# Kernel optimization log

Hardware: AMD Instinct MI355X
Metric: run time of the kernel (lower is better)

The kernel has to match this reference:

```python
import jax, jax.numpy as jnp
import numpy as np

# Hard-coded 36-node detector graph from the source (1-indexed), 220 directed edges.
E_SRC = [1,2,3,4,5,6,7,8,9,10,11,12,13,14,15,16,17,18,19,20,21,22,23,24,25,26,27,28,29,30,31,32,33,34,35,36,4,3,8,7,19,20,15,16,35,36,31,32,11,12,11,11,11,12,12,12,6,5,25,26,28,25,9,9,9,10,10,10,1,2,3,4,5,6,7,8,9,10,11,12,13,14,15,16,17,18,17,18,19,20,16,15,31,32,36,35,3,4,7,8,6,5,25,28,14,9,12,11,1,4,2,3,4,1,6,7,8,5,10,11,12,9,14,15,16,13,18,19,20,17,22,23,24,21,26,27,28,25,30,31,32,29,34,35,36,33,33,34,1,2,14,13,30,29,23,22,21,24,22,21,36,33,4,31,30,15,27,28,18,17,10,9,14,19,18,5,8,1,19,20,21,22,23,24,25,26,27,28,29,30,31,32,33,34,35,36,25,26,13,14,30,29,24,21,23,22,33,34,1,2,28,27,10,9,12,15,22,21,11,10]
E_DST = [2,3,4,1,6,7,8,5,10,11,12,9,14,15,16,13,18,19,20,17,22,23,24,21,26,27,28,25,30,31,32,29,34,35,36,33,33,34,1,2,14,13,30,29,23,22,21,24,22,21,36,33,4,31,30,15,27,28,18,17,10,9,14,19,18,5,8,1,19,20,21,22,23,24,25,26,27,28,29,30,31,32,33,34,35,36,25,26,13,14,30,29,24,21,23,22,33,34,1,2,28,27,10,9,12,15,22,21,11,10,1,2,3,4,5,6,7,8,9,10,11,12,13,14,15,16,17,18,19,20,21,22,23,24,25,26,27,28,29,30,31,32,33,34,35,36,4,3,8,7,19,20,15,16,35,36,31,32,11,12,11,11,11,12,12,12,6,5,25,26,28,25,9,9,9,10,10,10,1,2,3,4,5,6,7,8,9,10,11,12,13,14,15,16,17,18,17,18,19,20,16,15,31,32,36,35,3,4,7,8,6,5,25,28,14,9,12,11,1,4]

B = 20000   # graphs per batch
P = 36      # nodes per graph
N = B * P


def setup_inputs() -> dict:
    key = jax.random.key(0)
    ks = jax.random.split(key, 12)
    src = np.asarray(E_SRC, np.int32) - 1
    dst = np.asarray(E_DST, np.int32) - 1
    offs = (np.arange(B, dtype=np.int32) * P)[:, None]
    edge_index = jnp.asarray(np.stack([(src[None, :] + offs).reshape(-1),
                                       (dst[None, :] + offs).reshape(-1)]))  # [2, B*220]
    batch_index = jnp.asarray(np.repeat(np.arange(B, dtype=np.int32), P))  # [N]
    x = jax.random.normal(ks[0], (N, 2), jnp.float32)
    pos = jax.random.normal(ks[1], (N, 3), jnp.float32)  # unused by forward (faithful to source)

    def lin_w(k, fi, fo):
        s = 1.0 / np.sqrt(fi)
        return jax.random.uniform(k, (fi, fo), jnp.float32, -s, s)

    def lin_b(k, fo):
        return jax.random.uniform(k, (fo,), jnp.float32, -0.05, 0.05)

    return {
        "x": x, "edge_index": edge_index, "pos": pos, "batch_index": batch_index,
        "W0": lin_w(ks[2], 2, 4),   "b0": lin_b(ks[3], 4),
        "W1": lin_w(ks[4], 4, 12),  "b1": lin_b(ks[5], 12),
        "W2": lin_w(ks[6], 12, 16), "b2": lin_b(ks[7], 16),
        "W3": lin_w(ks[8], 16, 32), "b3": lin_b(ks[9], 32),
        "Wfc": lin_w(ks[10], 64, 7), "bfc": lin_b(ks[11], 7),
    }


def reference(x, edge_index, pos, batch_index, W0, b0, W1, b1, W2, b2, W3, b3, Wfc, bfc):
    del pos  # present in the torch signature but unused
    src, dst = edge_index[0], edge_index[1]
    n = x.shape[0]
    # GCN symmetric normalization with self-loops: deg = 1 + in-degree
    deg = jax.ops.segment_sum(jnp.ones(src.shape, x.dtype), dst, num_segments=n) + 1.0
    inv = deg ** -0.5
    enorm = inv[src] * inv[dst]   # edge norm
    snorm = inv * inv             # self-loop norm (deg^-1)

    def gcn_conv(h, W, b):
        h = h @ W  # [n, fo]
        agg = jax.ops.segment_sum(h[src] * enorm[:, None], dst, num_segments=n)
        return agg + h * snorm[:, None] + b

    h = jax.nn.relu(gcn_conv(x, W0, b0))
    h = jax.nn.relu(gcn_conv(h, W1, b1))
    # dropout(0.2) is identity in eval mode
    h = jax.nn.relu(gcn_conv(h, W2, b2))
    h = jax.nn.relu(gcn_conv(h, W3, b3))

    gmp = jax.ops.segment_max(h, batch_index, num_segments=B)
    counts = jax.ops.segment_sum(jnp.ones((n,), h.dtype), batch_index, num_segments=B)
    gap = jax.ops.segment_sum(h, batch_index, num_segments=B) / counts[:, None]
    hidden = jnp.concatenate([gmp, gap], axis=1)  # [B, 64]
    out = jax.nn.relu(hidden @ Wfc + bfc)         # [B, 7]
    return (out, hidden)
```

## Files before the change

### kernel.cpp

```cpp
#include <hip/hip_runtime.h>

typedef __attribute__((ext_vector_type(2))) float f32x2;
typedef __attribute__((ext_vector_type(4))) float f32x4;

#define NGRAPH 20000
#define GPT 7
#define STRIDE 36
#define SB (STRIDE * 4)
#define BSTREAM (GPT * 36 * STRIDE)
#define BSTREAMB (BSTREAM * 4)

static __constant__ int c_indeg[36] = {
    7,5,5,7,6,5,5,6,9,9,9,9,5,7,7,5,5,6,6,5,7,7,5,5,7,5,5,7,5,6,6,5,6,5,5,6
};
static __constant__ signed char c_adj[36][9] = {
    {3,7,9,6,1,18,10,0,0},      {0,6,7,2,19,0,0,0,0},
    {1,3,33,32,20,0,0,0,0},     {2,10,0,32,21,33,9,0,0},
    {7,9,5,27,22,26,0,0,0},     {4,6,26,23,27,0,0,0,0},
    {5,7,1,24,0,0,0,0,0},       {6,9,4,0,25,1,0,0,0},
    {11,24,27,9,13,18,17,26,14},{8,27,24,3,10,4,7,0,27},
    {9,0,11,21,35,32,3,28,20},  {10,13,8,20,30,29,14,29,21},
    {15,19,18,13,30,0,0,0,0},   {12,18,8,19,14,31,11,0,0},
    {13,11,8,15,29,32,28,0,0},  {14,12,28,33,29,0,0,0,0},
    {19,25,17,34,24,0,0,0,0},   {16,24,8,18,35,25,0,0,0},
    {17,8,0,19,13,12,0,0,0},    {18,1,16,12,13,0,0,0,0},
    {23,30,11,2,31,10,21,0,0},  {20,35,10,3,34,11,22,0,0},
    {21,34,4,35,23,0,0,0,0},    {22,31,5,30,20,0,0,0,0},
    {27,6,16,25,17,8,9,0,0},    {24,7,17,26,16,0,0,0,0},
    {25,5,8,27,4,0,0,0,0},      {26,4,9,5,24,9,8,0,0},
    {31,15,10,14,29,0,0,0,0},   {28,14,11,11,15,30,0,0,0},
    {29,11,12,31,20,23,0,0,0},  {30,13,28,23,20,0,0,0,0},
    {35,3,10,14,2,33,0,0,0},    {32,2,15,3,34,0,0,0,0},
    {33,16,35,22,21,0,0,0,0},   {34,10,17,32,21,22,0,0,0},
};
static __constant__ float c_inv[36] = {
    0.35355339f,0.40824829f,0.40824829f,0.35355339f,0.37796447f,0.40824829f,
    0.40824829f,0.37796447f,0.31622777f,0.31622777f,0.31622777f,0.31622777f,
    0.40824829f,0.35355339f,0.35355339f,0.40824829f,0.40824829f,0.37796447f,
    0.37796447f,0.40824829f,0.35355339f,0.35355339f,0.40824829f,0.40824829f,
    0.35355339f,0.40824829f,0.40824829f,0.35355339f,0.40824829f,0.37796447f,
    0.37796447f,0.40824829f,0.37796447f,0.40824829f,0.40824829f,0.37796447f,
};

static __device__ __forceinline__ f32x2 relu2(f32x2 v) {
    return __builtin_elementwise_max(v, (f32x2){0.f, 0.f});
}

static __device__ __forceinline__ void xf1(const float* a, const float* W1,
                                           const float* b1, f32x2* h) {
    f32x2 z[6];
    const f32x2* bv = (const f32x2*)b1;
#pragma unroll
    for (int j = 0; j < 6; ++j) z[j] = bv[j];
    const f32x2* Wv = (const f32x2*)W1;
#pragma unroll
    for (int i = 0; i < 4; ++i) {
        const f32x2 av = {a[i], a[i]};
#pragma unroll
        for (int j = 0; j < 6; ++j)
            z[j] = __builtin_elementwise_fma(av, Wv[i * 6 + j], z[j]);
    }
#pragma unroll
    for (int j = 0; j < 6; ++j) h[j] = relu2(z[j]);
}
static __device__ __forceinline__ void xf2(const float* a, const float* W2,
                                           const float* b2, f32x2* h) {
    f32x2 z[8];
    const f32x2* bv = (const f32x2*)b2;
#pragma unroll
    for (int j = 0; j < 8; ++j) z[j] = bv[j];
    const f32x2* Wv = (const f32x2*)W2;
#pragma unroll
    for (int i = 0; i < 12; ++i) {
        const f32x2 av = {a[i], a[i]};
#pragma unroll
        for (int j = 0; j < 8; ++j)
            z[j] = __builtin_elementwise_fma(av, Wv[i * 8 + j], z[j]);
    }
#pragma unroll
    for (int j = 0; j < 8; ++j) h[j] = relu2(z[j]);
}
static __device__ __forceinline__ void xf3(const float* a, const float* W3,
                                           const float* b3, f32x2* h) {
    f32x2 z[16];
    const f32x2* bv = (const f32x2*)b3;
#pragma unroll
    for (int j = 0; j < 16; ++j) z[j] = bv[j];
    const f32x2* Wv = (const f32x2*)W3;
#pragma unroll
    for (int i = 0; i < 16; ++i) {
        const f32x2 av = {a[i], a[i]};
#pragma unroll
        for (int j = 0; j < 16; ++j)
            z[j] = __builtin_elementwise_fma(av, Wv[i * 16 + j], z[j]);
    }
#pragma unroll
    for (int j = 0; j < 16; ++j) h[j] = relu2(z[j]);
}

extern "C" __global__ __launch_bounds__(256, 2)
void gcn_fused(const float* __restrict__ x,
               const float* __restrict__ W0, const float* __restrict__ b0,
               const float* __restrict__ W1, const float* __restrict__ b1,
               const float* __restrict__ W2, const float* __restrict__ b2,
               const float* __restrict__ W3, const float* __restrict__ b3,
               const float* __restrict__ Wfc, const float* __restrict__ bfc,
               float* __restrict__ out)
{
    __shared__ float L[2 * BSTREAM];

    const int t = threadIdx.x;
    const int g = t / 36;
    const int v = t - g * 36;
    const bool act = (g < GPT);
    const int gq = act ? g : GPT - 1;
    const int vc = act ? v : 0;
    const int GA = blockIdx.x * (2 * GPT) + g;
    const int GB = GA + GPT;
    const int GcA = (act && GA < NGRAPH) ? GA : 0;
    const int GcB = (act && GB < NGRAPH) ? GB : 0;
    const bool okB = (GB < NGRAPH);

    const int nd = c_indeg[vc];
    const float inv_v = c_inv[vc];
    int aoff[9], boff[9];
#pragma unroll
    for (int k = 0; k < 9; ++k) {
        aoff[k] = (gq * 36 + (int)c_adj[vc][k]) * SB;
        boff[k] = aoff[k] + BSTREAMB;
    }
    float* srowA = &L[(gq * 36 + vc) * STRIDE];
    float* srowB = srowA + BSTREAM;
    const char* Lb = (const char*)L;

    f32x2 h0A[2], h0B[2];
    {
        const float2* x2 = (const float2*)x;
        const float2 xA = x2[(size_t)GcA * 36 + vc];
        const float2 xB = x2[(size_t)GcB * 36 + vc];
        const f32x2 sA = {xA.x * inv_v, xA.y * inv_v};
        const f32x2 sB = {xB.x * inv_v, xB.y * inv_v};
        if (act) { *(f32x2*)&srowA[32] = sA; *(f32x2*)&srowB[32] = sB; }
        __syncthreads();
        f32x2 cA = sA, cB = sB;
#pragma unroll
        for (int k = 0; k < 5; ++k) {
            cA += *(const f32x2*)(Lb + aoff[k] + 128);
            cB += *(const f32x2*)(Lb + boff[k] + 128);
        }
        if (nd > 5) { cA += *(const f32x2*)(Lb + aoff[5] + 128);
                      cB += *(const f32x2*)(Lb + boff[5] + 128); }
        if (nd > 6) { cA += *(const f32x2*)(Lb + aoff[6] + 128);
                      cB += *(const f32x2*)(Lb + boff[6] + 128); }
        if (nd > 7) { cA += *(const f32x2*)(Lb + aoff[7] + 128);
                      cB += *(const f32x2*)(Lb + boff[7] + 128);
                      cA += *(const f32x2*)(Lb + aoff[8] + 128);
                      cB += *(const f32x2*)(Lb + boff[8] + 128); }
        const f32x2* W0v = (const f32x2*)W0;
        const f32x2* b0v = (const f32x2*)b0;
        {
            const float a0 = cA.x * inv_v, a1 = cA.y * inv_v;
            const f32x2 a0v = {a0, a0}, a1v = {a1, a1};
            h0A[0] = relu2(__builtin_elementwise_fma(a0v, W0v[0],
                     __builtin_elementwise_fma(a1v, W0v[2], b0v[0])));
            h0A[1] = relu2(__builtin_elementwise_fma(a0v, W0v[1],
                     __builtin_elementwise_fma(a1v, W0v[3], b0v[1])));
        }
        {
            const float a0 = cB.x * inv_v, a1 = cB.y * inv_v;
            const f32x2 a0v = {a0, a0}, a1v = {a1, a1};
            h0B[0] = relu2(__builtin_elementwise_fma(a0v, W0v[0],
                     __builtin_elementwise_fma(a1v, W0v[2], b0v[0])));
            h0B[1] = relu2(__builtin_elementwise_fma(a0v, W0v[1],
                     __builtin_elementwise_fma(a1v, W0v[3], b0v[1])));
        }
    }

    f32x2 h1A[6], h1B[6];
    {
        const f32x2 iv = {inv_v, inv_v};
        const f32x2 sA0 = h0A[0] * iv, sA1 = h0A[1] * iv;
        const f32x2 sB0 = h0B[0] * iv, sB1 = h0B[1] * iv;
        if (act) {
            *(f32x4*)&srowA[0] = (f32x4){sA0.x, sA0.y, sA1.x, sA1.y};
            *(f32x4*)&srowB[0] = (f32x4){sB0.x, sB0.y, sB1.x, sB1.y};
        }
        __syncthreads();
        f32x4 cA = {sA0.x, sA0.y, sA1.x, sA1.y};
        f32x4 cB = {sB0.x, sB0.y, sB1.x, sB1.y};
#pragma unroll
        for (int k = 0; k < 5; ++k) {
            cA += *(const f32x4*)(Lb + aoff[k]);
            cB += *(const f32x4*)(Lb + boff[k]);
        }
        if (nd > 5) { cA += *(const f32x4*)(Lb + aoff[5]);
                      cB += *(const f32x4*)(Lb + boff[5]); }
        if (nd > 6) { cA += *(const f32x4*)(Lb + aoff[6]);
                      cB += *(const f32x4*)(Lb + boff[6]); }
        if (nd > 7) { cA += *(const f32x4*)(Lb + aoff[7]);
                      cB += *(const f32x4*)(Lb + boff[7]);
                      cA += *(const f32x4*)(Lb + aoff[8]);
                      cB += *(const f32x4*)(Lb + boff[8]); }
        float aA[4], aB[4];
#pragma unroll
        for (int i = 0; i < 4; ++i) { aA[i] = cA[i] * inv_v; aB[i] = cB[i] * inv_v; }
        xf1(aA, W1, b1, h1A);
        xf1(aB, W1, b1, h1B);
    }

    f32x2 h2A[8], h2B[8];
    {
        const f32x2 iv = {inv_v, inv_v};
        f32x2 sA[6], sB[6];
#pragma unroll
        for (int j = 0; j < 6; ++j) { sA[j] = h1A[j] * iv; sB[j] = h1B[j] * iv; }
        if (act) {
            *(f32x4*)&srowA[4]  = (f32x4){sA[0].x, sA[0].y, sA[1].x, sA[1].y};
            *(f32x4*)&srowA[8]  = (f32x4){sA[2].x, sA[2].y, sA[3].x, sA[3].y};
            *(f32x4*)&srowA[12] = (f32x4){sA[4].x, sA[4].y, sA[5].x, sA[5].y};
            *(f32x4*)&srowB[4]  = (f32x4){sB[0].x, sB[0].y, sB[1].x, sB[1].y};
            *(f32x4*)&srowB[8]  = (f32x4){sB[2].x, sB[2].y, sB[3].x, sB[3].y};
            *(f32x4*)&srowB[12] = (f32x4){sB[4].x, sB[4].y, sB[5].x, sB[5].y};
        }
        __syncthreads();
        f32x4 cA0 = {sA[0].x, sA[0].y, sA[1].x, sA[1].y};
        f32x4 cA1 = {sA[2].x, sA[2].y, sA[3].x, sA[3].y};
        f32x4 cA2 = {sA[4].x, sA[4].y, sA[5].x, sA[5].y};
        f32x4 cB0 = {sB[0].x, sB[0].y, sB[1].x, sB[1].y};
        f32x4 cB1 = {sB[2].x, sB[2].y, sB[3].x, sB[3].y};
        f32x4 cB2 = {sB[4].x, sB[4].y, sB[5].x, sB[5].y};
#pragma unroll
        for (int k = 0; k < 5; ++k) {
            const char* pa = Lb + aoff[k] + 16;
            const char* pb = Lb + boff[k] + 16;
            cA0 += *(const f32x4*)(pa);      cB0 += *(const f32x4*)(pb);
            cA1 += *(const f32x4*)(pa + 16); cB1 += *(const f32x4*)(pb + 16);
            cA2 += *(const f32x4*)(pa + 32); cB2 += *(const f32x4*)(pb + 32);
        }
        if (nd > 5) { const char* pa = Lb + aoff[5] + 16; const char* pb = Lb + boff[5] + 16;
            cA0 += *(const f32x4*)(pa);      cB0 += *(const f32x4*)(pb);
            cA1 += *(const f32x4*)(pa + 16); cB1 += *(const f32x4*)(pb + 16);
            cA2 += *(const f32x4*)(pa + 32); cB2 += *(const f32x4*)(pb + 32); }
        if (nd > 6) { const char* pa = Lb + aoff[6] + 16; const char* pb = Lb + boff[6] + 16;
            cA0 += *(const f32x4*)(pa);      cB0 += *(const f32x4*)(pb);
            cA1 += *(const f32x4*)(pa + 16); cB1 += *(const f32x4*)(pb + 16);
            cA2 += *(const f32x4*)(pa + 32); cB2 += *(const f32x4*)(pb + 32); }
        if (nd > 7) {
            const char* pa = Lb + aoff[7] + 16; const char* pb = Lb + boff[7] + 16;
            cA0 += *(const f32x4*)(pa);      cB0 += *(const f32x4*)(pb);
            cA1 += *(const f32x4*)(pa + 16); cB1 += *(const f32x4*)(pb + 16);
            cA2 += *(const f32x4*)(pa + 32); cB2 += *(const f32x4*)(pb + 32);
            const char* qa = Lb + aoff[8] + 16; const char* qb = Lb + boff[8] + 16;
            cA0 += *(const f32x4*)(qa);      cB0 += *(const f32x4*)(qb);
            cA1 += *(const f32x4*)(qa + 16); cB1 += *(const f32x4*)(qb + 16);
            cA2 += *(const f32x4*)(qa + 32); cB2 += *(const f32x4*)(qb + 32);
        }
        float aA[12], aB[12];
#pragma unroll
        for (int i = 0; i < 4; ++i) {
            aA[i] = cA0[i] * inv_v; aA[4+i] = cA1[i] * inv_v; aA[8+i] = cA2[i] * inv_v;
            aB[i] = cB0[i] * inv_v; aB[4+i] = cB1[i] * inv_v; aB[8+i] = cB2[i] * inv_v;
        }
        xf2(aA, W2, b2, h2A);
        xf2(aB, W2, b2, h2B);
    }

    f32x2 h3A[16], h3B[16];
    {
        const f32x2 iv = {inv_v, inv_v};
        f32x2 sA[8], sB[8];
#pragma unroll
        for (int j = 0; j < 8; ++j) { sA[j] = h2A[j] * iv; sB[j] = h2B[j] * iv; }
        if (act) {
#pragma unroll
            for (int q = 0; q < 4; ++q) {
                *(f32x4*)&srowA[16 + q*4] =
                    (f32x4){sA[2*q].x, sA[2*q].y, sA[2*q+1].x, sA[2*q+1].y};
                *(f32x4*)&srowB[16 + q*4] =
                    (f32x4){sB[2*q].x, sB[2*q].y, sB[2*q+1].x, sB[2*q+1].y};
            }
        }
        __syncthreads();
        f32x4 cA0 = {sA[0].x, sA[0].y, sA[1].x, sA[1].y};
        f32x4 cA1 = {sA[2].x, sA[2].y, sA[3].x, sA[3].y};
        f32x4 cA2 = {sA[4].x, sA[4].y, sA[5].x, sA[5].y};
        f32x4 cA3 = {sA[6].x, sA[6].y, sA[7].x, sA[7].y};
        f32x4 cB0 = {sB[0].x, sB[0].y, sB[1].x, sB[1].y};
        f32x4 cB1 = {sB[2].x, sB[2].y, sB[3].x, sB[3].y};
        f32x4 cB2 = {sB[4].x, sB[4].y, sB[5].x, sB[5].y};
        f32x4 cB3 = {sB[6].x, sB[6].y, sB[7].x, sB[7].y};
#pragma unroll
        for (int k = 0; k < 5; ++k) {
            const char* pa = Lb + aoff[k] + 64;
            const char* pb = Lb + boff[k] + 64;
            cA0 += *(const f32x4*)(pa);      cB0 += *(const f32x4*)(pb);
            cA1 += *(const f32x4*)(pa + 16); cB1 += *(const f32x4*)(pb + 16);
            cA2 += *(const f32x4*)(pa + 32); cB2 += *(const f32x4*)(pb + 32);
            cA3 += *(const f32x4*)(pa + 48); cB3 += *(const f32x4*)(pb + 48);
        }
        if (nd > 5) { const char* pa = Lb + aoff[5] + 64; const char* pb = Lb + boff[5] + 64;
            cA0 += *(const f32x4*)(pa);      cB0 += *(const f32x4*)(pb);
            cA1 += *(const f32x4*)(pa + 16); cB1 += *(const f32x4*)(pb + 16);
            cA2 += *(const f32x4*)(pa + 32); cB2 += *(const f32x4*)(pb + 32);
            cA3 += *(const f32x4*)(pa + 48); cB3 += *(const f32x4*)(pb + 48); }
        if (nd > 6) { const char* pa = Lb + aoff[6] + 64; const char* pb = Lb + boff[6] + 64;
            cA0 += *(const f32x4*)(pa);      cB0 += *(const f32x4*)(pb);
            cA1 += *(const f32x4*)(pa + 16); cB1 += *(const f32x4*)(pb + 16);
            cA2 += *(const f32x4*)(pa + 32); cB2 += *(const f32x4*)(pb + 32);
            cA3 += *(const f32x4*)(pa + 48); cB3 += *(const f32x4*)(pb + 48); }
        if (nd > 7) {
            const char* pa = Lb + aoff[7] + 64; const char* pb = Lb + boff[7] + 64;
            cA0 += *(const f32x4*)(pa);      cB0 += *(const f32x4*)(pb);
            cA1 += *(const f32x4*)(pa + 16); cB1 += *(const f32x4*)(pb + 16);
            cA2 += *(const f32x4*)(pa + 32); cB2 += *(const f32x4*)(pb + 32);
            cA3 += *(const f32x4*)(pa + 48); cB3 += *(const f32x4*)(pb + 48);
            const char* qa = Lb + aoff[8] + 64; const char* qb = Lb + boff[8] + 64;
            cA0 += *(const f32x4*)(qa);      cB0 += *(const f32x4*)(qb);
            cA1 += *(const f32x4*)(qa + 16); cB1 += *(const f32x4*)(qb + 16);
            cA2 += *(const f32x4*)(qa + 32); cB2 += *(const f32x4*)(qb + 32);
            cA3 += *(const f32x4*)(qa + 48); cB3 += *(const f32x4*)(qb + 48);
        }
        float aA[16], aB[16];
#pragma unroll
        for (int i = 0; i < 4; ++i) {
            aA[i] = cA0[i] * inv_v; aA[4+i]  = cA1[i] * inv_v;
            aA[8+i] = cA2[i] * inv_v; aA[12+i] = cA3[i] * inv_v;
            aB[i] = cB0[i] * inv_v; aB[4+i]  = cB1[i] * inv_v;
            aB[8+i] = cB2[i] * inv_v; aB[12+i] = cB3[i] * inv_v;
        }
        xf3(aA, W3, b3, h3A);
        xf3(aB, W3, b3, h3B);
    }

    if (act) {
        *(f32x4*)&srowA[0] = (f32x4){h3A[0].x, h3A[0].y, h3A[1].x, h3A[1].y};
        *(f32x4*)&srowA[4] = (f32x4){h3A[2].x, h3A[2].y, h3A[3].x, h3A[3].y};
        *(f32x4*)&srowA[8] = (f32x4){h3A[4].x, h3A[4].y, h3A[5].x, h3A[5].y};
        *(f32x4*)&srowB[0] = (f32x4){h3B[0].x, h3B[0].y, h3B[1].x, h3B[1].y};
        *(f32x4*)&srowB[4] = (f32x4){h3B[2].x, h3B[2].y, h3B[3].x, h3B[3].y};
        *(f32x4*)&srowB[8] = (f32x4){h3B[4].x, h3B[4].y, h3B[5].x, h3B[5].y};
    }
    __syncthreads();
    if (act) {
#pragma unroll
        for (int q = 0; q < 5; ++q) {
            *(f32x4*)&srowA[12 + q*4] =
                (f32x4){h3A[6+2*q].x, h3A[6+2*q].y, h3A[7+2*q].x, h3A[7+2*q].y};
            *(f32x4*)&srowB[12 + q*4] =
                (f32x4){h3B[6+2*q].x, h3B[6+2*q].y, h3B[7+2*q].x, h3B[7+2*q].y};
        }
    }
    __syncthreads();

    if (t < GPT * 32) {
        const int pg = t >> 5, pf = t & 31;
        const int PA = blockIdx.x * (2 * GPT) + pg;
        const int PB = PA + GPT;
        const float* colA = &L[(pg * 36) * STRIDE + pf];
        const float* colB = colA + BSTREAM;
        float mxA = -1e30f, smA = 0.f, mxB = -1e30f, smB = 0.f;
#pragma unroll
        for (int u = 0; u < 36; ++u) {
            const float vA = colA[u * STRIDE];
            const float vB = colB[u * STRIDE];
            mxA = fmaxf(mxA, vA); smA += vA;
            mxB = fmaxf(mxB, vB); smB += vB;
        }
        const float gapA = smA * (1.0f / 36.0f);
        const float gapB = smB * (1.0f / 36.0f);
        {
            float* ho = out + (size_t)NGRAPH * 7 + (size_t)PA * 64;
            ho[pf] = mxA; ho[32 + pf] = gapA;
        }
        if (PB < NGRAPH) {
            float* ho = out + (size_t)NGRAPH * 7 + (size_t)PB * 64;
            ho[pf] = mxB; ho[32 + pf] = gapB;
        }
        float pA[7], pB[7];
        const float* wr0 = Wfc + pf * 7;
        const float* wr1 = Wfc + (32 + pf) * 7;
#pragma unroll
        for (int o = 0; o < 7; ++o) {
            pA[o] = fmaf(mxA, wr0[o], gapA * wr1[o]);
            pB[o] = fmaf(mxB, wr0[o], gapB * wr1[o]);
        }
#pragma unroll
        for (int m = 16; m >= 1; m >>= 1) {
#pragma unroll
            for (int o = 0; o < 7; ++o) {
                pA[o] += __shfl_xor(pA[o], m, 32);
                pB[o] += __shfl_xor(pB[o], m, 32);
            }
        }
        if (pf < 7) {
            float wA = pA[0], wB = pB[0];
            wA = (pf == 1) ? pA[1] : wA;  wB = (pf == 1) ? pB[1] : wB;
            wA = (pf == 2) ? pA[2] : wA;  wB = (pf == 2) ? pB[2] : wB;
            wA = (pf == 3) ? pA[3] : wA;  wB = (pf == 3) ? pB[3] : wB;
            wA = (pf == 4) ? pA[4] : wA;  wB = (pf == 4) ? pB[4] : wB;
            wA = (pf == 5) ? pA[5] : wA;  wB = (pf == 5) ? pB[5] : wB;
            wA = (pf == 6) ? pA[6] : wA;  wB = (pf == 6) ? pB[6] : wB;
            out[(size_t)PA * 7 + pf] = fmaxf(wA + bfc[pf], 0.f);
            if (PB < NGRAPH)
                out[(size_t)PB * 7 + pf] = fmaxf(wB + bfc[pf], 0.f);
        }
    }
}

extern "C" void kernel_launch(void* const* d_in, const int* in_sizes, int n_in,
                              void* d_out, int out_size, void* d_ws, size_t ws_size,
                              hipStream_t stream) {
    (void)in_sizes; (void)n_in; (void)d_ws; (void)ws_size; (void)out_size;
    const float* x   = (const float*)d_in[0];
    const float* W0  = (const float*)d_in[4];
    const float* b0  = (const float*)d_in[5];
    const float* W1  = (const float*)d_in[6];
    const float* b1  = (const float*)d_in[7];
    const float* W2  = (const float*)d_in[8];
    const float* b2  = (const float*)d_in[9];
    const float* W3  = (const float*)d_in[10];
    const float* b3  = (const float*)d_in[11];
    const float* Wfc = (const float*)d_in[12];
    const float* bfc = (const float*)d_in[13];
    float* out = (float*)d_out;

    const int nblocks = (NGRAPH + 2 * GPT - 1) / (2 * GPT);
    hipLaunchKernelGGL(gcn_fused, dim3(nblocks), dim3(256), 0, stream,
                       x, W0, b0, W1, b1, W2, b2, W3, b3, Wfc, bfc, out);
}
```

Measured before the change: 40.99 us.

## Shrink blocks to one wavefront handling two graphs each

Blocks go from 256 threads covering 14 graphs to 64 threads (one wavefront) covering 2 graphs, with 10000 blocks launched and launch bounds set to 64,4. This removes the 256-thread block that left 4 lanes idle and lets __syncthreads act within a single wave, which makes barriers cheap and avoids the bounds checks. The cost is 28 of 64 lanes idle during the node phases (only 36 nodes), many more small blocks to schedule, and much lower shared memory per block. The pooling phase now uses all 64 lanes, one half-wave per graph.

```diff
diff --git a/kernel.cpp b/kernel.cpp
--- a/kernel.cpp
+++ b/kernel.cpp
@@ -4,10 +4,9 @@
 typedef __attribute__((ext_vector_type(4))) float f32x4;
 
 #define NGRAPH 20000
-#define GPT 7
 #define STRIDE 36
 #define SB (STRIDE * 4)
-#define BSTREAM (GPT * 36 * STRIDE)
+#define BSTREAM (36 * STRIDE)
 #define BSTREAMB (BSTREAM * 4)
 
 static __constant__ int c_indeg[36] = {
@@ -98,7 +97,7 @@
     for (int j = 0; j < 16; ++j) h[j] = relu2(z[j]);
 }
 
-extern "C" __global__ __launch_bounds__(256, 2)
+extern "C" __global__ __launch_bounds__(64, 4)
 void gcn_fused(const float* __restrict__ x,
                const float* __restrict__ W0, const float* __restrict__ b0,
                const float* __restrict__ W1, const float* __restrict__ b1,
@@ -110,34 +109,28 @@
     __shared__ float L[2 * BSTREAM];
 
     const int t = threadIdx.x;
-    const int g = t / 36;
-    const int v = t - g * 36;
-    const bool act = (g < GPT);
-    const int gq = act ? g : GPT - 1;
-    const int vc = act ? v : 0;
-    const int GA = blockIdx.x * (2 * GPT) + g;
-    const int GB = GA + GPT;
-    const int GcA = (act && GA < NGRAPH) ? GA : 0;
-    const int GcB = (act && GB < NGRAPH) ? GB : 0;
-    const bool okB = (GB < NGRAPH);
+    const bool act = (t < 36);
+    const int vc = act ? t : 0;
+    const int GA = blockIdx.x * 2;
+    const int GB = GA + 1;
 
     const int nd = c_indeg[vc];
     const float inv_v = c_inv[vc];
     int aoff[9], boff[9];
 #pragma unroll
     for (int k = 0; k < 9; ++k) {
-        aoff[k] = (gq * 36 + (int)c_adj[vc][k]) * SB;
+        aoff[k] = (int)c_adj[vc][k] * SB;
         boff[k] = aoff[k] + BSTREAMB;
     }
-    float* srowA = &L[(gq * 36 + vc) * STRIDE];
+    float* srowA = &L[vc * STRIDE];
     float* srowB = srowA + BSTREAM;
     const char* Lb = (const char*)L;
 
     f32x2 h0A[2], h0B[2];
     {
         const float2* x2 = (const float2*)x;
-        const float2 xA = x2[(size_t)GcA * 36 + vc];
-        const float2 xB = x2[(size_t)GcB * 36 + vc];
+        const float2 xA = x2[(size_t)GA * 36 + vc];
+        const float2 xB = x2[(size_t)GB * 36 + vc];
         const f32x2 sA = {xA.x * inv_v, xA.y * inv_v};
         const f32x2 sB = {xB.x * inv_v, xB.y * inv_v};
         if (act) { *(f32x2*)&srowA[32] = sA; *(f32x2*)&srowB[32] = sB; }
@@ -352,57 +345,42 @@
     }
     __syncthreads();
 
-    if (t < GPT * 32) {
-        const int pg = t >> 5, pf = t & 31;
-        const int PA = blockIdx.x * (2 * GPT) + pg;
-        const int PB = PA + GPT;
-        const float* colA = &L[(pg * 36) * STRIDE + pf];
-        const float* colB = colA + BSTREAM;
-        float mxA = -1e30f, smA = 0.f, mxB = -1e30f, smB = 0.f;
+    {
+        const int ph = t >> 5;
+        const int pf = t & 31;
+        const int PG = GA + ph;
+        const float* col = &L[ph * BSTREAM + pf];
+        float mx = -1e30f, sm = 0.f;
 #pragma unroll
         for (int u = 0; u < 36; ++u) {
-            const float vA = colA[u * STRIDE];
-            const float vB = colB[u * STRIDE];
-            mxA = fmaxf(mxA, vA); smA += vA;
-            mxB = fmaxf(mxB, vB); smB += vB;
-        }
-        const float gapA = smA * (1.0f / 36.0f);
-        const float gapB = smB * (1.0f / 36.0f);
-        {
-            float* ho = out + (size_t)NGRAPH * 7 + (size_t)PA * 64;
-            ho[pf] = mxA; ho[32 + pf] = gapA;
-        }
-        if (PB < NGRAPH) {
-            float* ho = out + (size_t)NGRAPH * 7 + (size_t)PB * 64;
-            ho[pf] = mxB; ho[32 + pf] = gapB;
-        }
-        float pA[7], pB[7];
+            const float val = col[u * STRIDE];
+            mx = fmaxf(mx, val); sm += val;
+        }
+        const float gap = sm * (1.0f / 36.0f);
+        float* ho = out + (size_t)NGRAPH * 7 + (size_t)PG * 64;
+        ho[pf] = mx; ho[32 + pf] = gap;
+
+        float p[7];
         const float* wr0 = Wfc + pf * 7;
         const float* wr1 = Wfc + (32 + pf) * 7;
 #pragma unroll
-        for (int o = 0; o < 7; ++o) {
-            pA[o] = fmaf(mxA, wr0[o], gapA * wr1[o]);
-            pB[o] = fmaf(mxB, wr0[o], gapB * wr1[o]);
-        }
+        for (int o = 0; o < 7; ++o)
+            p[o] = fmaf(mx, wr0[o], gap * wr1[o]);
 #pragma unroll
         for (int m = 16; m >= 1; m >>= 1) {
 #pragma unroll
-            for (int o = 0; o < 7; ++o) {
-                pA[o] += __shfl_xor(pA[o], m, 32);
-                pB[o] += __shfl_xor(pB[o], m, 32);
-            }
+            for (int o = 0; o < 7; ++o)
+                p[o] += __shfl_xor(p[o], m, 32);
         }
         if (pf < 7) {
-            float wA = pA[0], wB = pB[0];
-            wA = (pf == 1) ? pA[1] : wA;  wB = (pf == 1) ? pB[1] : wB;
-            wA = (pf == 2) ? pA[2] : wA;  wB = (pf == 2) ? pB[2] : wB;
-            wA = (pf == 3) ? pA[3] : wA;  wB = (pf == 3) ? pB[3] : wB;
-            wA = (pf == 4) ? pA[4] : wA;  wB = (pf == 4) ? pB[4] : wB;
-            wA = (pf == 5) ? pA[5] : wA;  wB = (pf == 5) ? pB[5] : wB;
-            wA = (pf == 6) ? pA[6] : wA;  wB = (pf == 6) ? pB[6] : wB;
-            out[(size_t)PA * 7 + pf] = fmaxf(wA + bfc[pf], 0.f);
-            if (PB < NGRAPH)
-                out[(size_t)PB * 7 + pf] = fmaxf(wB + bfc[pf], 0.f);
+            float w = p[0];
+            w = (pf == 1) ? p[1] : w;
+            w = (pf == 2) ? p[2] : w;
+            w = (pf == 3) ? p[3] : w;
+            w = (pf == 4) ? p[4] : w;
+            w = (pf == 5) ? p[5] : w;
+            w = (pf == 6) ? p[6] : w;
+            out[(size_t)PG * 7 + pf] = fmaxf(w + bfc[pf], 0.f);
         }
     }
 }
@@ -424,7 +402,7 @@
     const float* bfc = (const float*)d_in[13];
     float* out = (float*)d_out;
 
-    const int nblocks = (NGRAPH + 2 * GPT - 1) / (2 * GPT);
-    hipLaunchKernelGGL(gcn_fused, dim3(nblocks), dim3(256), 0, stream,
+    const int nblocks = NGRAPH / 2;
+    hipLaunchKernelGGL(gcn_fused, dim3(nblocks), dim3(64), 0, stream,
                        x, W0, b0, W1, b1, W2, b2, W3, b3, Wfc, bfc, out);
 }
```

After: 44.82 us. 1.09x slower.
